# Optimization experiments

Hardware: AMD Instinct MI355X
Metric: run time of the kernel (lower is better)

The kernel has to match this reference:

```python
import jax, jax.numpy as jnp
import numpy as np

# Conv / KAN hyperparameters (from init_kwargs)
KH, KW = 3, 3
SH, SW = 1, 1
FILTERS = 128
GRID_SIZE = 5
SPLINE_ORDER = 3
GRID_RANGE = (-1.0, 1.0)
B, H, W, C = 16, 64, 64, 32
IN_SIZE = KH * KW * C                      # 288
BASIS = GRID_SIZE + SPLINE_ORDER           # 8


def make_grid():
    a, b = GRID_RANGE
    h = (b - a) / GRID_SIZE
    pts = a + h * jnp.arange(-SPLINE_ORDER, GRID_SIZE + SPLINE_ORDER + 1, dtype=jnp.float32)
    return jnp.tile(pts[None, :], (IN_SIZE, 1))   # (in_size, grid_size+2*order+1) = (288, 12)


def extract_patches(x):
    # TF tf.image.extract_patches ordering: flattened as (kh, kw, C)
    Bx, Hx, Wx, Cx = x.shape
    oh = (Hx - KH) // SH + 1
    ow = (Wx - KW) // SW + 1
    slices = []
    for di in range(KH):
        for dj in range(KW):
            slices.append(x[:, di:di + SH * oh:SH, dj:dj + SW * ow:SW, :])
    return jnp.concatenate(slices, axis=-1)        # (B, oh, ow, KH*KW*C)


def bspline_basis(x, grid):
    # x: (N, D), grid: (D, G) -> (N, D, G-1-order) via Cox-de Boor recursion
    x = x[..., None]
    bases = ((x >= grid[:, :-1]) & (x < grid[:, 1:])).astype(x.dtype)
    for k in range(1, SPLINE_ORDER + 1):
        left = (x - grid[:, :-(k + 1)]) / (grid[:, k:-1] - grid[:, :-(k + 1)])
        right = (grid[:, k + 1:] - x) / (grid[:, k + 1:] - grid[:, 1:-k])
        bases = left * bases[..., :-1] + right * bases[..., 1:]
    return bases


def setup_inputs() -> dict:
    key = jax.random.key(0)
    k1, k2, k3 = jax.random.split(key, 3)
    inputs = jax.random.uniform(k1, (B, H, W, C), dtype=jnp.float32,
                                minval=GRID_RANGE[0], maxval=GRID_RANGE[1])
    spline_kernel = 0.1 * jax.random.normal(k2, (IN_SIZE, BASIS, FILTERS), dtype=jnp.float32)
    scale_factor = 1.0 + 0.05 * jax.random.normal(k3, (IN_SIZE, FILTERS), dtype=jnp.float32)
    bias = jnp.zeros((FILTERS,), dtype=jnp.float32)
    grid = make_grid()
    return {"inputs": inputs, "spline_kernel": spline_kernel,
            "scale_factor": scale_factor, "bias": bias, "grid": grid}


def reference(inputs, spline_kernel, scale_factor, bias, grid):
    patches = extract_patches(inputs)                       # (B, oh, ow, in_size)
    Bx, oh, ow, D = patches.shape
    p2 = patches.reshape(-1, D)                             # (N, in_size)
    bases = bspline_basis(p2, grid)                         # (N, in_size, basis)
    # Faithful to tfkan DenseKAN: out = sum_i scale[i,o] * (spline_i(x_i)[o] + silu(x_i))
    # fused so the (N, in_size, units) intermediate is never materialized.
    w = spline_kernel * scale_factor[:, None, :]            # (in_size, basis, units)
    out = jnp.einsum('nik,iko->no', bases, w)               # spline part
    out = out + jax.nn.silu(p2) @ scale_factor              # base-activation part
    out = out.reshape(Bx, oh, ow, FILTERS) + bias
    return out
```

## Files before the change

kernel.cpp:

```cpp
#include <hip/hip_runtime.h>
#include <stdint.h>


typedef int   i32x4 __attribute__((ext_vector_type(4)));
typedef __attribute__((address_space(1))) const uint32_t gu32;
typedef __attribute__((address_space(3))) uint32_t lu32;

#define ABI8_BYTES  20971520u
#define WT2I8_BYTES 368640u
#define B_BUF       8192
#define GEMM_LDS    (2 * B_BUF)

__device__ __forceinline__ uint32_t q8(float v, float s) {
  int q = (int)rintf(v * s);
  q = q > 127 ? 127 : (q < -127 ? -127 : q);
  return (uint32_t)(uint8_t)(int8_t)q;
}

__device__ __forceinline__ void bspline9(float x, float slot[9]) {
  float t  = (x + 1.f) * 2.5f;
  float ff = floorf(t);
  ff = fminf(fmaxf(ff, 0.f), 4.f);
  int   f  = (int)ff;
  float u  = t - ff;
  float um = 1.f - u;
  float u2 = u * u, u3 = u2 * u;
  float w0 = um * um * um * (1.f / 6.f);
  float w1 = (3.f * u3 - 6.f * u2 + 4.f) * (1.f / 6.f);
  float w2 = (-3.f * u3 + 3.f * u2 + 3.f * u + 1.f) * (1.f / 6.f);
  float w3 = u3 * (1.f / 6.f);
#pragma unroll
  for (int k = 0; k < 8; ++k) {
    int d = k - f;
    slot[k] = (d == 0) ? w0 : (d == 1) ? w1 : (d == 2) ? w2 : (d == 3) ? w3 : 0.f;
  }
  slot[8] = x / (1.f + __expf(-x));
}

__global__ void kan_wmax(const float* __restrict__ sk, const float* __restrict__ sc,
                         float* __restrict__ wscale, float* __restrict__ oscale) {
  __shared__ float red[256];
  const int f = blockIdx.x, tid = threadIdx.x;
  float m = 1e-8f;
  for (int i = tid; i < 288; i += 256) {
    float s = fabsf(sc[i * 128 + f]);
    m = fmaxf(m, s);
#pragma unroll
    for (int ks = 0; ks < 8; ++ks)
      m = fmaxf(m, fabsf(sk[(i * 8 + ks) * 128 + f]) * s);
  }
  red[tid] = m;
  __syncthreads();
  for (int w = 128; w > 0; w >>= 1) {
    if (tid < w) red[tid] = fmaxf(red[tid], red[tid + w]);
    __syncthreads();
  }
  if (tid == 0) {
    wscale[f] = 127.f / red[0];
    oscale[f] = red[0] / (127.f * 127.f);
  }
}

__global__ void kan_prep(const float* __restrict__ in,
                         const float* __restrict__ sk,
                         const float* __restrict__ sc,
                         const float* __restrict__ wscale,
                         char* __restrict__ AbI8, char* __restrict__ Wt2I8) {
  const int tid = threadIdx.x, bid = blockIdx.x;
  if (bid < 1024) {
    int idx = bid * 256 + tid;
    int px = idx >> 2, g8 = idx & 3;
    const float* ip = in + (uint32_t)px * 32u + g8 * 8;
    float4 x0 = *reinterpret_cast<const float4*>(ip);
    float4 x1 = *reinterpret_cast<const float4*>(ip + 4);
    float s[8][9];
    bspline9(x0.x, s[0]); bspline9(x0.y, s[1]);
    bspline9(x0.z, s[2]); bspline9(x0.w, s[3]);
    bspline9(x1.x, s[4]); bspline9(x1.y, s[5]);
    bspline9(x1.z, s[6]); bspline9(x1.w, s[7]);
    char* row = AbI8 + (uint32_t)px * 320u + (uint32_t)g8 * 8u;
#pragma unroll
    for (int ks = 0; ks < 9; ++ks) {
      uint32_t lo = 0, hi = 0;
#pragma unroll
      for (int j = 0; j < 4; ++j) {
        lo |= q8(s[j][ks], 127.f) << (8 * j);
        hi |= q8(s[4 + j][ks], 127.f) << (8 * j);
      }
      uint2 pk; pk.x = lo; pk.y = hi;
      *reinterpret_cast<uint2*>(row + ks * 32) = pk;
    }
    uint2 z; z.x = 0; z.y = 0;
    *reinterpret_cast<uint2*>(row + 9 * 32) = z;
  } else {
    int t = (bid - 1024) * 256 + tid;
    int f  = t & 127;
    int kb = (t >> 7) * 16;
    float ws = wscale[f];
    uint32_t w[4] = {0u, 0u, 0u, 0u};
#pragma unroll
    for (int e = 0; e < 16; ++e) {
      int k = kb + e;
      int dd = k / 320, r = k - dd * 320;
      int slot = r >> 5, c = r & 31;
      int i = dd * 32 + c;
      float v = 0.f;
      if (slot < 8)       v = sk[(i * 8 + slot) * 128 + f] * sc[i * 128 + f];
      else if (slot == 8) v = sc[i * 128 + f];
      w[e >> 2] |= q8(v, ws) << (8 * (e & 3));
    }
    uint4 pk; pk.x = w[0]; pk.y = w[1]; pk.z = w[2]; pk.w = w[3];
    *reinterpret_cast<uint4*>(Wt2I8 + (uint32_t)t * 16u) = pk;
  }
}

#define WAITBAR0 asm volatile("s_waitcnt vmcnt(0)\n\ts_barrier" ::: "memory")

__global__ __launch_bounds__(256, 2)
void kan_gemm(const char* __restrict__ AbI8, const char* __restrict__ Wt2I8,
              const float* __restrict__ bias, const float* __restrict__ oscale,
              float* __restrict__ out) {
  extern __shared__ __align__(16) char smem[];
  const int tid = threadIdx.x;
  const int wave = tid >> 6, lane = tid & 63;
  const int l15 = lane & 15, l4 = lane >> 4;

  const int orig = blockIdx.x;
  const int xcd = orig & 7, i8 = orig >> 3;
  const int wg = (xcd < 1 ? xcd * 61 : 61 + (xcd - 1) * 60) + i8;
  const int m0 = wg * 128;

  const char* Abase[2];
#pragma unroll
  for (int mi = 0; mi < 2; ++mi) {
    int opix = m0 + wave * 32 + mi * 16 + l15;
    if (opix > 61503) opix = 61503;
    int b = opix / 3844, rem = opix - b * 3844;
    int oy = rem / 62, ox = rem - oy * 62;
    uint32_t ipix = (uint32_t)(b * 4096 + oy * 64 + ox);
    Abase[mi] = AbI8 + ipix * 320u + (uint32_t)l4 * 16u;
  }
  const char* sB = Wt2I8 + (uint32_t)wave * 2048u + (uint32_t)lane * 16u;

  float bvv[8], os[8];
#pragma unroll
  for (int ni = 0; ni < 8; ++ni) {
    bvv[ni] = bias[ni * 16 + l15];
    os[ni]  = oscale[ni * 16 + l15];
  }
  asm volatile("s_waitcnt vmcnt(0)" ::: "memory");

  i32x4 acc[2][8];
#pragma unroll
  for (int mi = 0; mi < 2; ++mi)
#pragma unroll
    for (int ni = 0; ni < 8; ++ni)
      acc[mi][ni] = (i32x4){0, 0, 0, 0};

#define BSTAGE(buf, tq)                                                        \
  { _Pragma("unroll") for (int j = 0; j < 2; ++j)                              \
      __builtin_amdgcn_global_load_lds(                                        \
          (gu32*)(sB + (uint32_t)(tq) * 8192u + j * 1024),                     \
          (lu32*)(smem + (buf) * B_BUF + wave * 2048 + j * 1024), 16, 0, 0); }

#define AGATHER(dst, tq)                                                       \
  { const int dd = (tq) / 5, s5 = (tq) - dd * 5;                               \
    const int di = dd / 3;                                                     \
    const int eo = (di * 64 + (dd - di * 3)) * 320 + s5 * 64;                  \
    _Pragma("unroll") for (int mi = 0; mi < 2; ++mi)                           \
      dst[mi] = *reinterpret_cast<const i32x4*>(Abase[mi] + eo); }

#define STEP(t_, bufc, avC, avN)                                               \
  {                                                                            \
    WAITBAR0;                      \
    { const int tn = ((t_) + 1 <= 44) ? (t_) + 1 : 44;                         \
      AGATHER(avN, tn)                                                         \
      BSTAGE((bufc) ^ 1, tn) }                                                 \
    const char* Bp = smem + (bufc) * B_BUF;                                    \
    i32x4 bv[8];                                                               \
    _Pragma("unroll") for (int ni = 0; ni < 8; ++ni)                           \
      bv[ni] = *reinterpret_cast<const i32x4*>(                                \
          Bp + l4 * 2048 + (ni * 16 + l15) * 16);                              \
    __builtin_amdgcn_s_setprio(1);                                             \
    _Pragma("unroll") for (int mi = 0; mi < 2; ++mi)                           \
    _Pragma("unroll") for (int ni = 0; ni < 8; ++ni)                           \
      acc[mi][ni] = __builtin_amdgcn_mfma_i32_16x16x64_i8(                     \
          avC[mi], bv[ni], acc[mi][ni], 0, 0, 0);                              \
    __builtin_amdgcn_s_setprio(0);                                             \
  }

  i32x4 avA[2], avB[2];
  AGATHER(avA, 0)
  BSTAGE(0, 0)

#pragma unroll 1
  for (int t = 0; t < 44; t += 2) {
    STEP(t, 0, avA, avB)
    STEP(t + 1, 1, avB, avA)
  }
  STEP(44, 0, avA, avB)

#pragma unroll
  for (int mi = 0; mi < 2; ++mi) {
#pragma unroll
    for (int ni = 0; ni < 8; ++ni) {
#pragma unroll
      for (int j = 0; j < 4; ++j) {
        int p = m0 + wave * 32 + mi * 16 + l4 * 4 + j;
        if (p < 61504)
          out[(uint64_t)p * 128 + ni * 16 + l15] =
              (float)acc[mi][ni][j] * os[ni] + bvv[ni];
      }
    }
  }
}

extern "C" void kernel_launch(void* const* d_in, const int* in_sizes, int n_in,
                              void* d_out, int out_size, void* d_ws, size_t ws_size,
                              hipStream_t stream) {
  const float* inp  = (const float*)d_in[0];
  const float* sk   = (const float*)d_in[1];
  const float* sc   = (const float*)d_in[2];
  const float* bias = (const float*)d_in[3];
  float* out = (float*)d_out;

  char*  AbI8   = (char*)d_ws;
  char*  Wt2I8  = (char*)d_ws + ABI8_BYTES;
  float* wscale = (float*)((char*)d_ws + ABI8_BYTES + WT2I8_BYTES);
  float* oscale = wscale + 128;

  hipFuncSetAttribute((const void*)kan_gemm,
                      hipFuncAttributeMaxDynamicSharedMemorySize, GEMM_LDS);

  kan_wmax<<<dim3(128), dim3(256), 0, stream>>>(sk, sc, wscale, oscale);
  kan_prep<<<dim3(1024 + 90), dim3(256), 0, stream>>>(inp, sk, sc, wscale, AbI8, Wt2I8);
  kan_gemm<<<dim3(481), dim3(256), GEMM_LDS, stream>>>(AbI8, Wt2I8, bias, oscale, out);
}
```

Baseline: 63.38 us.

## Fuse weight-max reduction into prep kernel and stage activation writes through LDS

Removes the separate kan_wmax launch by giving each filter its own block in kan_prep. That block computes the fused weights, reduces their max in shared memory, then quantizes and writes them. The activation half now builds each block's 20 KB int8 tile in LDS and copies it out with coalesced 16-byte stores, replacing scattered 8-byte global writes. This saves one kernel launch and its serialization, but adds a block barrier and LDS traffic. The weight-block writes are strided by filter, which may be less coalesced.

```diff
diff --git a/kernel.cpp b/kernel.cpp
--- a/kernel.cpp
+++ b/kernel.cpp
@@ -37,40 +37,17 @@
   slot[8] = x / (1.f + __expf(-x));
 }
 
-__global__ void kan_wmax(const float* __restrict__ sk, const float* __restrict__ sc,
-                         float* __restrict__ wscale, float* __restrict__ oscale) {
-  __shared__ float red[256];
-  const int f = blockIdx.x, tid = threadIdx.x;
-  float m = 1e-8f;
-  for (int i = tid; i < 288; i += 256) {
-    float s = fabsf(sc[i * 128 + f]);
-    m = fmaxf(m, s);
-#pragma unroll
-    for (int ks = 0; ks < 8; ++ks)
-      m = fmaxf(m, fabsf(sk[(i * 8 + ks) * 128 + f]) * s);
-  }
-  red[tid] = m;
-  __syncthreads();
-  for (int w = 128; w > 0; w >>= 1) {
-    if (tid < w) red[tid] = fmaxf(red[tid], red[tid + w]);
-    __syncthreads();
-  }
-  if (tid == 0) {
-    wscale[f] = 127.f / red[0];
-    oscale[f] = red[0] / (127.f * 127.f);
-  }
-}
-
 __global__ void kan_prep(const float* __restrict__ in,
                          const float* __restrict__ sk,
                          const float* __restrict__ sc,
-                         const float* __restrict__ wscale,
-                         char* __restrict__ AbI8, char* __restrict__ Wt2I8) {
+                         char* __restrict__ AbI8, char* __restrict__ Wt2I8,
+                         float* __restrict__ oscale) {
+  __shared__ __align__(16) char lds[20480];
   const int tid = threadIdx.x, bid = blockIdx.x;
   if (bid < 1024) {
-    int idx = bid * 256 + tid;
-    int px = idx >> 2, g8 = idx & 3;
-    const float* ip = in + (uint32_t)px * 32u + g8 * 8;
+    int pxl = tid >> 2, g8 = tid & 3;
+    uint32_t px = (uint32_t)bid * 64u + (uint32_t)pxl;
+    const float* ip = in + px * 32u + g8 * 8;
     float4 x0 = *reinterpret_cast<const float4*>(ip);
     float4 x1 = *reinterpret_cast<const float4*>(ip + 4);
     float s[8][9];
@@ -78,7 +55,7 @@
     bspline9(x0.z, s[2]); bspline9(x0.w, s[3]);
     bspline9(x1.x, s[4]); bspline9(x1.y, s[5]);
     bspline9(x1.z, s[6]); bspline9(x1.w, s[7]);
-    char* row = AbI8 + (uint32_t)px * 320u + (uint32_t)g8 * 8u;
+    char* row = lds + pxl * 320 + g8 * 8;
 #pragma unroll
     for (int ks = 0; ks < 9; ++ks) {
       uint32_t lo = 0, hi = 0;
@@ -92,25 +69,50 @@
     }
     uint2 z; z.x = 0; z.y = 0;
     *reinterpret_cast<uint2*>(row + 9 * 32) = z;
+    __syncthreads();
+    const uint4* ls = reinterpret_cast<const uint4*>(lds);
+    uint4* gd = reinterpret_cast<uint4*>(AbI8 + (uint32_t)bid * 20480u);
+#pragma unroll
+    for (int j = 0; j < 5; ++j) gd[tid + j * 256] = ls[tid + j * 256];
   } else {
-    int t = (bid - 1024) * 256 + tid;
-    int f  = t & 127;
-    int kb = (t >> 7) * 16;
-    float ws = wscale[f];
-    uint32_t w[4] = {0u, 0u, 0u, 0u};
-#pragma unroll
-    for (int e = 0; e < 16; ++e) {
-      int k = kb + e;
-      int dd = k / 320, r = k - dd * 320;
-      int slot = r >> 5, c = r & 31;
-      int i = dd * 32 + c;
-      float v = 0.f;
-      if (slot < 8)       v = sk[(i * 8 + slot) * 128 + f] * sc[i * 128 + f];
-      else if (slot == 8) v = sc[i * 128 + f];
-      w[e >> 2] |= q8(v, ws) << (8 * (e & 3));
-    }
-    uint4 pk; pk.x = w[0]; pk.y = w[1]; pk.z = w[2]; pk.w = w[3];
-    *reinterpret_cast<uint4*>(Wt2I8 + (uint32_t)t * 16u) = pk;
+    const int f = bid - 1024;
+    float w[16];
+    float m = 1e-8f;
+    const bool have = tid < 180;
+    if (have) {
+      int kb = tid * 16;
+#pragma unroll
+      for (int e = 0; e < 16; ++e) {
+        int k = kb + e;
+        int dd = k / 320, r = k - dd * 320;
+        int slot = r >> 5, c = r & 31;
+        int i = dd * 32 + c;
+        float v = 0.f;
+        if (slot < 8)       v = sk[(i * 8 + slot) * 128 + f] * sc[i * 128 + f];
+        else if (slot == 8) v = sc[i * 128 + f];
+        w[e] = v;
+        m = fmaxf(m, fabsf(v));
+      }
+    }
+    float* red = reinterpret_cast<float*>(lds);
+    red[tid] = m;
+    __syncthreads();
+    for (int s2 = 128; s2 > 0; s2 >>= 1) {
+      if (tid < s2) red[tid] = fmaxf(red[tid], red[tid + s2]);
+      __syncthreads();
+    }
+    const float mx = red[0];
+    if (tid == 0) oscale[f] = mx / (127.f * 127.f);
+    if (have) {
+      const float ws = 127.f / mx;
+      uint32_t p[4] = {0u, 0u, 0u, 0u};
+#pragma unroll
+      for (int e = 0; e < 16; ++e) p[e >> 2] |= q8(w[e], ws) << (8 * (e & 3));
+      uint4 pk; pk.x = p[0]; pk.y = p[1]; pk.z = p[2]; pk.w = p[3];
+      int sub = tid >> 2, chunk = tid & 3;
+      *reinterpret_cast<uint4*>(Wt2I8 + (uint32_t)sub * 8192u +
+                                (uint32_t)chunk * 2048u + (uint32_t)f * 16u) = pk;
+    }
   }
 }
 
@@ -226,13 +228,11 @@
 
   char*  AbI8   = (char*)d_ws;
   char*  Wt2I8  = (char*)d_ws + ABI8_BYTES;
-  float* wscale = (float*)((char*)d_ws + ABI8_BYTES + WT2I8_BYTES);
-  float* oscale = wscale + 128;
+  float* oscale = (float*)((char*)d_ws + ABI8_BYTES + WT2I8_BYTES);
 
   hipFuncSetAttribute((const void*)kan_gemm,
                       hipFuncAttributeMaxDynamicSharedMemorySize, GEMM_LDS);
 
-  kan_wmax<<<dim3(128), dim3(256), 0, stream>>>(sk, sc, wscale, oscale);
-  kan_prep<<<dim3(1024 + 90), dim3(256), 0, stream>>>(inp, sk, sc, wscale, AbI8, Wt2I8);
+  kan_prep<<<dim3(1024 + 128), dim3(256), 0, stream>>>(inp, sk, sc, AbI8, Wt2I8, oscale);
   kan_gemm<<<dim3(481), dim3(256), GEMM_LDS, stream>>>(AbI8, Wt2I8, bias, oscale, out);
 }
```

Result: faster. 56.61 us, median of 2 (-10.7%).
